# Optimization experiments

Measured on AMD Instinct MI355X. Metric: run time of the kernel, lower is better.

## Reference

```python
import jax, jax.numpy as jnp
import numpy as np

T, B, IN_DIM = 1024, 8, 512
D_VALUE, D_KEY = 64, 64
V_TH = 1.0
EPS = 1e-08


def setup_inputs() -> dict:
    key = jax.random.key(0)
    ks = jax.random.split(key, 7)
    s_in = 1.0 / np.sqrt(IN_DIM)
    x = jax.random.normal(ks[0], (T, B, IN_DIM), dtype=jnp.float32)
    Wv = jax.random.uniform(ks[1], (D_VALUE, IN_DIM), jnp.float32, -s_in, s_in)
    bv = jax.random.uniform(ks[2], (D_VALUE,), jnp.float32, -s_in, s_in)
    Wk = jax.random.uniform(ks[3], (D_KEY, IN_DIM), jnp.float32, -s_in, s_in)
    bk = jax.random.uniform(ks[4], (D_KEY,), jnp.float32, -s_in, s_in)
    Wa = jax.random.uniform(ks[5], (D_KEY, IN_DIM), jnp.float32, -s_in, s_in)
    ba = jax.random.uniform(ks[6], (D_KEY,), jnp.float32, -s_in, s_in)
    return {"x": x, "Wv": Wv, "bv": bv, "Wk": Wk, "bk": bk, "Wa": Wa, "ba": ba}


def reference(x, Wv, bv, Wk, bk, Wa, ba):
    # projections: v (T,B,d), k (T,B,n), alpha (T,B,n)
    v = jnp.einsum('tbi,di->tbd', x, Wv) + bv
    k = jnp.einsum('tbi,ni->tbn', x, Wk) + bk
    alpha = jax.nn.sigmoid(jnp.einsum('tbi,ni->tbn', x, Wa) + ba)
    # outer-product writes: (T,B,d,n)
    writes = jnp.einsum('tbd,tbn->tbdn', v, k)
    # closed-form linear recurrence S_t = S_{t-1} * alpha_t + writes_t via cumprod/cumsum
    P = jnp.cumprod(alpha, axis=0)                       # (T,B,n)
    invP = 1.0 / (P + EPS)
    scaled = writes * invP[:, :, None, :]                # (T,B,d,n)
    S = jnp.cumsum(scaled, axis=0) * P[:, :, None, :]    # (T,B,d,n)
    Tt, Bb = x.shape[0], x.shape[1]
    mem = S.reshape(Tt, Bb, D_VALUE * D_KEY)
    spk = (mem > V_TH).astype(mem.dtype)
    return spk, mem
```

## Files before the change

### kernel.cpp

```cpp
#include <hip/hip_runtime.h>
#include <cmath>

#define TT 1024
#define BB 8
#define IND 512
#define NCHUNK 32
#define CHLEN 32
#define EPSV 1e-8
#define OUTHALF ((size_t)TT * BB * 4096)

__global__ __launch_bounds__(256)
void k1_proj(const float* __restrict__ x,
             const float* __restrict__ Wv, const float* __restrict__ bv,
             const float* __restrict__ Wk, const float* __restrict__ bk,
             const float* __restrict__ Wa, const float* __restrict__ ba,
             float* __restrict__ vOut, float* __restrict__ kOut,
             double* __restrict__ aOut)
{
    __shared__ float sWt[64][192];
    __shared__ float sXt[64][16];
    const int tid = threadIdx.x;
    const int rowbase = blockIdx.x * 16;
    const int c0 = tid & 63;
    const int r0 = (tid >> 6) << 2;
    double a0[4] = {0,0,0,0}, a1[4] = {0,0,0,0}, a2[4] = {0,0,0,0};

    for (int ko = 0; ko < IND; ko += 64) {
        __syncthreads();
        if (tid < 192) {
            const float* src;
            if (tid < 64)       src = Wv + (size_t)tid * IND;
            else if (tid < 128) src = Wk + (size_t)(tid - 64) * IND;
            else                src = Wa + (size_t)(tid - 128) * IND;
            src += ko;
            #pragma unroll
            for (int q = 0; q < 64; q += 4) {
                float4 w4 = *(const float4*)(src + q);
                sWt[q+0][tid] = w4.x; sWt[q+1][tid] = w4.y;
                sWt[q+2][tid] = w4.z; sWt[q+3][tid] = w4.w;
            }
        }
        {
            int r  = tid & 15;
            int kq = (tid >> 4) << 2;
            float4 x4 = *(const float4*)(x + (size_t)(rowbase + r) * IND + ko + kq);
            sXt[kq+0][r] = x4.x; sXt[kq+1][r] = x4.y;
            sXt[kq+2][r] = x4.z; sXt[kq+3][r] = x4.w;
        }
        __syncthreads();

        float f0[4] = {0,0,0,0}, f1[4] = {0,0,0,0}, f2[4] = {0,0,0,0};
        #pragma unroll
        for (int q = 0; q < 64; ++q) {
            float4 xv = *(const float4*)&sXt[q][r0];
            float w0 = sWt[q][c0], w1 = sWt[q][c0 + 64], w2 = sWt[q][c0 + 128];
            f0[0] = fmaf(xv.x, w0, f0[0]); f1[0] = fmaf(xv.x, w1, f1[0]); f2[0] = fmaf(xv.x, w2, f2[0]);
            f0[1] = fmaf(xv.y, w0, f0[1]); f1[1] = fmaf(xv.y, w1, f1[1]); f2[1] = fmaf(xv.y, w2, f2[1]);
            f0[2] = fmaf(xv.z, w0, f0[2]); f1[2] = fmaf(xv.z, w1, f1[2]); f2[2] = fmaf(xv.z, w2, f2[2]);
            f0[3] = fmaf(xv.w, w0, f0[3]); f1[3] = fmaf(xv.w, w1, f1[3]); f2[3] = fmaf(xv.w, w2, f2[3]);
        }
        #pragma unroll
        for (int i = 0; i < 4; ++i) { a0[i] += f0[i]; a1[i] += f1[i]; a2[i] += f2[i]; }
    }

    #pragma unroll
    for (int i = 0; i < 4; ++i) {
        int r = rowbase + r0 + i;
        vOut[r * 64 + c0] = (float)(a0[i] + (double)bv[c0]);
        kOut[r * 64 + c0] = (float)(a1[i] + (double)bk[c0]);
        double z = a2[i] + (double)ba[c0];
        aOut[r * 64 + c0] = 1.0 / (1.0 + exp(-z));
    }
}

__global__ __launch_bounds__(256)
void k2a_chunkprod(const double* __restrict__ alpha, double* __restrict__ cpA)
{
    int gt = blockIdx.x * 256 + threadIdx.x;
    int ch = gt >> 9, chain = gt & 511;
    int b = chain >> 6, n = chain & 63;
    double p = 1.0;
    int base = ((ch * CHLEN) * BB + b) * 64 + n;
    for (int i = 0; i < CHLEN; ++i) p *= alpha[base + i * 512];
    cpA[gt] = p;
}

__global__ __launch_bounds__(512)
void k2b_prefix(double* __restrict__ cpA)
{
    int chain = threadIdx.x;
    double run = 1.0;
    for (int ch = 0; ch < NCHUNK; ++ch) {
        double t = cpA[ch * 512 + chain];
        cpA[ch * 512 + chain] = run;
        run *= t;
    }
}

__global__ __launch_bounds__(256)
void k3_csum(const float* __restrict__ vIn, const float* __restrict__ kIn,
             const double* __restrict__ alpha, const double* __restrict__ cpA,
             double* __restrict__ Csum)
{
    __shared__ double sV[CHLEN * 64];
    const int tid = threadIdx.x;
    const int ch = blockIdx.x >> 3;
    const int b  = blockIdx.x & 7;
    #pragma unroll
    for (int q = 0; q < 8; ++q) {
        int idx = q * 256 + tid;
        int ti = idx >> 6, d = idx & 63;
        sV[idx] = (double)vIn[(((ch * CHLEN + ti) * BB) + b) * 64 + d];
    }
    __syncthreads();
    const int n = tid & 63;
    const int w = tid >> 6;
    double P = cpA[ch * 512 + b * 64 + n];
    double C[16];
    #pragma unroll
    for (int j = 0; j < 16; ++j) C[j] = 0.0;
    for (int i = 0; i < CHLEN; ++i) {
        int base = ((ch * CHLEN + i) * BB + b) * 64 + n;
        P *= alpha[base];
        double invp = 1.0 / (P + EPSV);
        double kd = (double)kIn[base] * invp;
        const double* vrow = &sV[i * 64 + w * 16];
        #pragma unroll
        for (int j = 0; j < 16; ++j) C[j] = fma(vrow[j], kd, C[j]);
    }
    size_t cb = ((size_t)ch * 8 + b) * 4096 + (size_t)w * 1024 + n;
    #pragma unroll
    for (int j = 0; j < 16; ++j) Csum[cb + j * 64] = C[j];
}

__global__ __launch_bounds__(256)
void k3b_prefix(double* __restrict__ Csum)
{
    int s = blockIdx.x * 256 + threadIdx.x;
    int b = s >> 12, rest = s & 4095;
    double run = 0.0;
    for (int ch = 0; ch < NCHUNK; ++ch) {
        size_t idx = ((size_t)ch * 8 + b) * 4096 + rest;
        double t = Csum[idx];
        Csum[idx] = run;
        run += t;
    }
}

__global__ __launch_bounds__(256)
void k4_scan(const float* __restrict__ vIn, const float* __restrict__ kIn,
             const double* __restrict__ alpha, const double* __restrict__ cpA,
             const double* __restrict__ Csum, float* __restrict__ outp)
{
    __shared__ double sV[CHLEN * 64];
    const int tid = threadIdx.x;
    const int ch = blockIdx.x >> 3;
    const int b  = blockIdx.x & 7;
    #pragma unroll
    for (int q = 0; q < 8; ++q) {
        int idx = q * 256 + tid;
        int ti = idx >> 6, d = idx & 63;
        sV[idx] = (double)vIn[(((ch * CHLEN + ti) * BB) + b) * 64 + d];
    }
    __syncthreads();
    const int n = tid & 63;
    const int w = tid >> 6;
    double P = cpA[ch * 512 + b * 64 + n];
    size_t cb = ((size_t)ch * 8 + b) * 4096 + (size_t)w * 1024 + n;
    double C[16];
    #pragma unroll
    for (int j = 0; j < 16; ++j) C[j] = Csum[cb + j * 64];

    float* spk = outp;
    float* mem = outp + OUTHALF;
    for (int i = 0; i < CHLEN; ++i) {
        int t = ch * CHLEN + i;
        int base = (t * BB + b) * 64 + n;
        P *= alpha[base];
        double invp = 1.0 / (P + EPSV);
        double kd = (double)kIn[base] * invp;
        double vd[16];
        const double* vrow = &sV[i * 64 + w * 16];
        #pragma unroll
        for (int j = 0; j < 16; ++j) vd[j] = vrow[j];
        size_t ob = ((size_t)t * BB + b) * 4096 + (size_t)w * 1024 + n;
        #pragma unroll
        for (int j = 0; j < 16; ++j) {
            C[j] = fma(vd[j], kd, C[j]);
            double S = P * C[j];
            mem[ob + j * 64] = (float)S;
            spk[ob + j * 64] = (S > 1.0) ? 1.0f : 0.0f;
        }
    }
}

extern "C" void kernel_launch(void* const* d_in, const int* in_sizes, int n_in,
                              void* d_out, int out_size, void* d_ws, size_t ws_size,
                              hipStream_t stream)
{
    const float* x  = (const float*)d_in[0];
    const float* Wv = (const float*)d_in[1];
    const float* bv = (const float*)d_in[2];
    const float* Wk = (const float*)d_in[3];
    const float* bk = (const float*)d_in[4];
    const float* Wa = (const float*)d_in[5];
    const float* ba = (const float*)d_in[6];
    float* out = (float*)d_out;

    char* ws = (char*)d_ws;
    float*  v     = (float*)(ws);
    float*  kk    = (float*)(ws + (2u << 20));
    double* alpha = (double*)(ws + (4u << 20));
    double* cpA   = (double*)(ws + (8u << 20));
    double* Csum  = (double*)(ws + (8u << 20) + (1u << 17));

    hipLaunchKernelGGL(k1_proj,      dim3(512), dim3(256), 0, stream,
                       x, Wv, bv, Wk, bk, Wa, ba, v, kk, alpha);
    hipLaunchKernelGGL(k2a_chunkprod, dim3(64), dim3(256), 0, stream, alpha, cpA);
    hipLaunchKernelGGL(k2b_prefix,    dim3(1),  dim3(512), 0, stream, cpA);
    hipLaunchKernelGGL(k3_csum,       dim3(256), dim3(256), 0, stream,
                       v, kk, alpha, cpA, Csum);
    hipLaunchKernelGGL(k3b_prefix,    dim3(128), dim3(256), 0, stream, Csum);
    hipLaunchKernelGGL(k4_scan,       dim3(256), dim3(256), 0, stream,
                       v, kk, alpha, cpA, Csum, out);
}
```

Baseline: 117.9 us.

## Precompute per-step P and k/P arrays; drop single-block prefix kernel; enlarge projection tile

```diff
diff --git a/kernel.cpp b/kernel.cpp
--- a/kernel.cpp
+++ b/kernel.cpp
@@ -4,8 +4,8 @@
 #define TT 1024
 #define BB 8
 #define IND 512
-#define NCHUNK 32
-#define CHLEN 32
+#define NCH 32
+#define CHL 32
 #define EPSV 1e-8
 #define OUTHALF ((size_t)TT * BB * 4096)
 
@@ -18,21 +18,19 @@
              double* __restrict__ aOut)
 {
     __shared__ float sWt[64][192];
-    __shared__ float sXt[64][16];
+    __shared__ float sXt[64][32];
     const int tid = threadIdx.x;
-    const int rowbase = blockIdx.x * 16;
+    const int rowbase = blockIdx.x * 32;
     const int c0 = tid & 63;
-    const int r0 = (tid >> 6) << 2;
-    double a0[4] = {0,0,0,0}, a1[4] = {0,0,0,0}, a2[4] = {0,0,0,0};
+    const int r0 = (tid >> 6) << 3;
+    double av[8] = {}, ak[8] = {}, aa[8] = {};
 
     for (int ko = 0; ko < IND; ko += 64) {
         __syncthreads();
         if (tid < 192) {
-            const float* src;
-            if (tid < 64)       src = Wv + (size_t)tid * IND;
-            else if (tid < 128) src = Wk + (size_t)(tid - 64) * IND;
-            else                src = Wa + (size_t)(tid - 128) * IND;
-            src += ko;
+            const float* src = (tid < 64  ? Wv + (size_t)tid * IND
+                              : tid < 128 ? Wk + (size_t)(tid - 64) * IND
+                              :             Wa + (size_t)(tid - 128) * IND) + ko;
             #pragma unroll
             for (int q = 0; q < 64; q += 4) {
                 float4 w4 = *(const float4*)(src + q);
@@ -41,34 +39,40 @@
             }
         }
         {
-            int r  = tid & 15;
-            int kq = (tid >> 4) << 2;
-            float4 x4 = *(const float4*)(x + (size_t)(rowbase + r) * IND + ko + kq);
-            sXt[kq+0][r] = x4.x; sXt[kq+1][r] = x4.y;
-            sXt[kq+2][r] = x4.z; sXt[kq+3][r] = x4.w;
+            const int r  = tid & 31;
+            const int kq = (tid >> 5) << 3;
+            const float* xs = x + (size_t)(rowbase + r) * IND + ko + kq;
+            float4 xa = *(const float4*)xs;
+            float4 xb = *(const float4*)(xs + 4);
+            sXt[kq+0][r] = xa.x; sXt[kq+1][r] = xa.y; sXt[kq+2][r] = xa.z; sXt[kq+3][r] = xa.w;
+            sXt[kq+4][r] = xb.x; sXt[kq+5][r] = xb.y; sXt[kq+6][r] = xb.z; sXt[kq+7][r] = xb.w;
         }
         __syncthreads();
 
-        float f0[4] = {0,0,0,0}, f1[4] = {0,0,0,0}, f2[4] = {0,0,0,0};
+        float fv[8] = {}, fk[8] = {}, fa[8] = {};
         #pragma unroll
         for (int q = 0; q < 64; ++q) {
-            float4 xv = *(const float4*)&sXt[q][r0];
+            float4 xa = *(const float4*)&sXt[q][r0];
+            float4 xb = *(const float4*)&sXt[q][r0 + 4];
+            float xr[8] = {xa.x, xa.y, xa.z, xa.w, xb.x, xb.y, xb.z, xb.w};
             float w0 = sWt[q][c0], w1 = sWt[q][c0 + 64], w2 = sWt[q][c0 + 128];
-            f0[0] = fmaf(xv.x, w0, f0[0]); f1[0] = fmaf(xv.x, w1, f1[0]); f2[0] = fmaf(xv.x, w2, f2[0]);
-            f0[1] = fmaf(xv.y, w0, f0[1]); f1[1] = fmaf(xv.y, w1, f1[1]); f2[1] = fmaf(xv.y, w2, f2[1]);
-            f0[2] = fmaf(xv.z, w0, f0[2]); f1[2] = fmaf(xv.z, w1, f1[2]); f2[2] = fmaf(xv.z, w2, f2[2]);
-            f0[3] = fmaf(xv.w, w0, f0[3]); f1[3] = fmaf(xv.w, w1, f1[3]); f2[3] = fmaf(xv.w, w2, f2[3]);
-        }
-        #pragma unroll
-        for (int i = 0; i < 4; ++i) { a0[i] += f0[i]; a1[i] += f1[i]; a2[i] += f2[i]; }
-    }
-
-    #pragma unroll
-    for (int i = 0; i < 4; ++i) {
-        int r = rowbase + r0 + i;
-        vOut[r * 64 + c0] = (float)(a0[i] + (double)bv[c0]);
-        kOut[r * 64 + c0] = (float)(a1[i] + (double)bk[c0]);
-        double z = a2[i] + (double)ba[c0];
+            #pragma unroll
+            for (int j = 0; j < 8; ++j) {
+                fv[j] = fmaf(xr[j], w0, fv[j]);
+                fk[j] = fmaf(xr[j], w1, fk[j]);
+                fa[j] = fmaf(xr[j], w2, fa[j]);
+            }
+        }
+        #pragma unroll
+        for (int j = 0; j < 8; ++j) { av[j] += fv[j]; ak[j] += fk[j]; aa[j] += fa[j]; }
+    }
+
+    #pragma unroll
+    for (int j = 0; j < 8; ++j) {
+        size_t r = (size_t)rowbase + r0 + j;
+        vOut[r * 64 + c0] = (float)(av[j] + (double)bv[c0]);
+        kOut[r * 64 + c0] = (float)(ak[j] + (double)bk[c0]);
+        double z = aa[j] + (double)ba[c0];
         aOut[r * 64 + c0] = 1.0 / (1.0 + exp(-z));
     }
 }
@@ -78,31 +82,35 @@
 {
     int gt = blockIdx.x * 256 + threadIdx.x;
     int ch = gt >> 9, chain = gt & 511;
-    int b = chain >> 6, n = chain & 63;
     double p = 1.0;
-    int base = ((ch * CHLEN) * BB + b) * 64 + n;
-    for (int i = 0; i < CHLEN; ++i) p *= alpha[base + i * 512];
+    int base = (ch * CHL) * 512 + chain;
+    for (int i = 0; i < CHL; ++i) p *= alpha[base + i * 512];
     cpA[gt] = p;
 }
 
-__global__ __launch_bounds__(512)
-void k2b_prefix(double* __restrict__ cpA)
-{
-    int chain = threadIdx.x;
-    double run = 1.0;
-    for (int ch = 0; ch < NCHUNK; ++ch) {
-        double t = cpA[ch * 512 + chain];
-        cpA[ch * 512 + chain] = run;
-        run *= t;
-    }
-}
-
-__global__ __launch_bounds__(256)
-void k3_csum(const float* __restrict__ vIn, const float* __restrict__ kIn,
-             const double* __restrict__ alpha, const double* __restrict__ cpA,
+__global__ __launch_bounds__(256)
+void kP_scan(const float* __restrict__ kIn, const double* __restrict__ alpha,
+             const double* __restrict__ cpA,
+             double* __restrict__ Parr, double* __restrict__ kdArr)
+{
+    int gt = blockIdx.x * 256 + threadIdx.x;
+    int ch = gt >> 9, chain = gt & 511;
+    double P = 1.0;
+    for (int c = 0; c < ch; ++c) P *= cpA[c * 512 + chain];
+    int base = (ch * CHL) * 512 + chain;
+    for (int i = 0; i < CHL; ++i) {
+        int idx = base + i * 512;
+        P *= alpha[idx];
+        Parr[idx] = P;
+        kdArr[idx] = (double)kIn[idx] / (P + EPSV);
+    }
+}
+
+__global__ __launch_bounds__(256)
+void k3_csum(const float* __restrict__ vIn, const double* __restrict__ kdArr,
              double* __restrict__ Csum)
 {
-    __shared__ double sV[CHLEN * 64];
+    __shared__ double sV[CHL * 64];
     const int tid = threadIdx.x;
     const int ch = blockIdx.x >> 3;
     const int b  = blockIdx.x & 7;
@@ -110,20 +118,16 @@
     for (int q = 0; q < 8; ++q) {
         int idx = q * 256 + tid;
         int ti = idx >> 6, d = idx & 63;
-        sV[idx] = (double)vIn[(((ch * CHLEN + ti) * BB) + b) * 64 + d];
+        sV[idx] = (double)vIn[(((ch * CHL + ti) * BB) + b) * 64 + d];
     }
     __syncthreads();
     const int n = tid & 63;
     const int w = tid >> 6;
-    double P = cpA[ch * 512 + b * 64 + n];
     double C[16];
     #pragma unroll
     for (int j = 0; j < 16; ++j) C[j] = 0.0;
-    for (int i = 0; i < CHLEN; ++i) {
-        int base = ((ch * CHLEN + i) * BB + b) * 64 + n;
-        P *= alpha[base];
-        double invp = 1.0 / (P + EPSV);
-        double kd = (double)kIn[base] * invp;
+    for (int i = 0; i < CHL; ++i) {
+        double kd = kdArr[((ch * CHL + i) * BB + b) * 64 + n];
         const double* vrow = &sV[i * 64 + w * 16];
         #pragma unroll
         for (int j = 0; j < 16; ++j) C[j] = fma(vrow[j], kd, C[j]);
@@ -139,7 +143,7 @@
     int s = blockIdx.x * 256 + threadIdx.x;
     int b = s >> 12, rest = s & 4095;
     double run = 0.0;
-    for (int ch = 0; ch < NCHUNK; ++ch) {
+    for (int ch = 0; ch < NCH; ++ch) {
         size_t idx = ((size_t)ch * 8 + b) * 4096 + rest;
         double t = Csum[idx];
         Csum[idx] = run;
@@ -148,11 +152,11 @@
 }
 
 __global__ __launch_bounds__(256)
-void k4_scan(const float* __restrict__ vIn, const float* __restrict__ kIn,
-             const double* __restrict__ alpha, const double* __restrict__ cpA,
-             const double* __restrict__ Csum, float* __restrict__ outp)
-{
-    __shared__ double sV[CHLEN * 64];
+void k4_scan(const float* __restrict__ vIn, const double* __restrict__ kdArr,
+             const double* __restrict__ Parr, const double* __restrict__ Csum,
+             float* __restrict__ outp)
+{
+    __shared__ double sV[CHL * 64];
     const int tid = threadIdx.x;
     const int ch = blockIdx.x >> 3;
     const int b  = blockIdx.x & 7;
@@ -160,12 +164,11 @@
     for (int q = 0; q < 8; ++q) {
         int idx = q * 256 + tid;
         int ti = idx >> 6, d = idx & 63;
-        sV[idx] = (double)vIn[(((ch * CHLEN + ti) * BB) + b) * 64 + d];
+        sV[idx] = (double)vIn[(((ch * CHL + ti) * BB) + b) * 64 + d];
     }
     __syncthreads();
     const int n = tid & 63;
     const int w = tid >> 6;
-    double P = cpA[ch * 512 + b * 64 + n];
     size_t cb = ((size_t)ch * 8 + b) * 4096 + (size_t)w * 1024 + n;
     double C[16];
     #pragma unroll
@@ -173,20 +176,16 @@
 
     float* spk = outp;
     float* mem = outp + OUTHALF;
-    for (int i = 0; i < CHLEN; ++i) {
-        int t = ch * CHLEN + i;
+    for (int i = 0; i < CHL; ++i) {
+        int t = ch * CHL + i;
         int base = (t * BB + b) * 64 + n;
-        P *= alpha[base];
-        double invp = 1.0 / (P + EPSV);
-        double kd = (double)kIn[base] * invp;
-        double vd[16];
+        double kd = kdArr[base];
+        double P  = Parr[base];
         const double* vrow = &sV[i * 64 + w * 16];
-        #pragma unroll
-        for (int j = 0; j < 16; ++j) vd[j] = vrow[j];
         size_t ob = ((size_t)t * BB + b) * 4096 + (size_t)w * 1024 + n;
         #pragma unroll
         for (int j = 0; j < 16; ++j) {
-            C[j] = fma(vd[j], kd, C[j]);
+            C[j] = fma(vrow[j], kd, C[j]);
             double S = P * C[j];
             mem[ob + j * 64] = (float)S;
             spk[ob + j * 64] = (S > 1.0) ? 1.0f : 0.0f;
@@ -209,18 +208,21 @@
 
     char* ws = (char*)d_ws;
     float*  v     = (float*)(ws);
-    float*  kk    = (float*)(ws + (2u << 20));
-    double* alpha = (double*)(ws + (4u << 20));
-    double* cpA   = (double*)(ws + (8u << 20));
-    double* Csum  = (double*)(ws + (8u << 20) + (1u << 17));
-
-    hipLaunchKernelGGL(k1_proj,      dim3(512), dim3(256), 0, stream,
+    float*  kk    = (float*)(ws + ( 2u << 20));
+    double* alpha = (double*)(ws + ( 4u << 20));
+    double* cpA   = (double*)(ws + ( 8u << 20));
+    double* Parr  = (double*)(ws + ( 9u << 20));
+    double* kdArr = (double*)(ws + (13u << 20));
+    double* Csum  = (double*)(ws + (17u << 20));
+
+    hipLaunchKernelGGL(k1_proj,       dim3(256), dim3(256), 0, stream,
                        x, Wv, bv, Wk, bk, Wa, ba, v, kk, alpha);
-    hipLaunchKernelGGL(k2a_chunkprod, dim3(64), dim3(256), 0, stream, alpha, cpA);
-    hipLaunchKernelGGL(k2b_prefix,    dim3(1),  dim3(512), 0, stream, cpA);
+    hipLaunchKernelGGL(k2a_chunkprod, dim3(64),  dim3(256), 0, stream, alpha, cpA);
+    hipLaunchKernelGGL(kP_scan,       dim3(64),  dim3(256), 0, stream,
+                       kk, alpha, cpA, Parr, kdArr);
     hipLaunchKernelGGL(k3_csum,       dim3(256), dim3(256), 0, stream,
-                       v, kk, alpha, cpA, Csum);
+                       v, kdArr, Csum);
     hipLaunchKernelGGL(k3b_prefix,    dim3(128), dim3(256), 0, stream, Csum);
     hipLaunchKernelGGL(k4_scan,       dim3(256), dim3(256), 0, stream,
-                       v, kk, alpha, cpA, Csum, out);
-}
+                       v, kdArr, Parr, Csum, out);
+}
```

New measurement: 130.3 us. 1.11x slower.

## Fuse all stages into one cooperative kernel with grid syncs

Applied to the files above, without the earlier changes.

```diff
diff --git a/kernel.cpp b/kernel.cpp
--- a/kernel.cpp
+++ b/kernel.cpp
@@ -1,21 +1,174 @@
 #include <hip/hip_runtime.h>
+#include <hip/hip_cooperative_groups.h>
 #include <cmath>
 
 #define TT 1024
 #define BB 8
 #define IND 512
-#define NCHUNK 32
-#define CHLEN 32
+#define NCH 32
+#define CHL 32
 #define EPSV 1e-8
 #define OUTHALF ((size_t)TT * BB * 4096)
 
-__global__ __launch_bounds__(256)
-void k1_proj(const float* __restrict__ x,
-             const float* __restrict__ Wv, const float* __restrict__ bv,
-             const float* __restrict__ Wk, const float* __restrict__ bk,
-             const float* __restrict__ Wa, const float* __restrict__ ba,
-             float* __restrict__ vOut, float* __restrict__ kOut,
-             double* __restrict__ aOut)
+namespace cg = cooperative_groups;
+
+
+union SharedMem {
+    struct { float Wt[32][192]; float Xt[32][16]; } g;
+    struct { double A[CHL][64]; double V[CHL][32]; float K[CHL][64]; } s;
+};
+
+__global__ __launch_bounds__(256, 2)
+void mega(const float* __restrict__ x,
+          const float* __restrict__ Wv, const float* __restrict__ bv,
+          const float* __restrict__ Wk, const float* __restrict__ bk,
+          const float* __restrict__ Wa, const float* __restrict__ ba,
+          float* __restrict__ vBuf, float* __restrict__ kBuf,
+          double* __restrict__ aBuf, double* __restrict__ cpA,
+          double* __restrict__ Csum, float* __restrict__ outp)
+{
+    cg::grid_group grid = cg::this_grid();
+    __shared__ SharedMem sh;
+    const int tid = threadIdx.x;
+    const int bid = blockIdx.x;
+
+    {
+        const int rowbase = bid * 16;
+        const int c0 = tid & 63;
+        const int r0 = (tid >> 6) << 2;
+        double av[4] = {}, ak[4] = {}, aa[4] = {};
+
+        for (int ko = 0; ko < IND; ko += 32) {
+            __syncthreads();
+            if (tid < 192) {
+                const float* src = (tid < 64  ? Wv + (size_t)tid * IND
+                                  : tid < 128 ? Wk + (size_t)(tid - 64) * IND
+                                  :             Wa + (size_t)(tid - 128) * IND) + ko;
+                #pragma unroll
+                for (int q = 0; q < 32; q += 4) {
+                    float4 w4 = *(const float4*)(src + q);
+                    sh.g.Wt[q+0][tid] = w4.x; sh.g.Wt[q+1][tid] = w4.y;
+                    sh.g.Wt[q+2][tid] = w4.z; sh.g.Wt[q+3][tid] = w4.w;
+                }
+            }
+            {
+                int r  = tid & 15;
+                int kq = (tid >> 4) << 1;
+                float2 x2 = *(const float2*)(x + (size_t)(rowbase + r) * IND + ko + kq);
+                sh.g.Xt[kq][r] = x2.x; sh.g.Xt[kq+1][r] = x2.y;
+            }
+            __syncthreads();
+
+            float fv[4] = {}, fk[4] = {}, fa[4] = {};
+            #pragma unroll
+            for (int q = 0; q < 32; ++q) {
+                float4 xa = *(const float4*)&sh.g.Xt[q][r0];
+                float xr[4] = {xa.x, xa.y, xa.z, xa.w};
+                float w0 = sh.g.Wt[q][c0], w1 = sh.g.Wt[q][c0 + 64], w2 = sh.g.Wt[q][c0 + 128];
+                #pragma unroll
+                for (int j = 0; j < 4; ++j) {
+                    fv[j] = fmaf(xr[j], w0, fv[j]);
+                    fk[j] = fmaf(xr[j], w1, fk[j]);
+                    fa[j] = fmaf(xr[j], w2, fa[j]);
+                }
+            }
+            #pragma unroll
+            for (int j = 0; j < 4; ++j) { av[j] += fv[j]; ak[j] += fk[j]; aa[j] += fa[j]; }
+        }
+        #pragma unroll
+        for (int j = 0; j < 4; ++j) {
+            size_t r = (size_t)rowbase + r0 + j;
+            vBuf[r * 64 + c0] = (float)(av[j] + (double)bv[c0]);
+            kBuf[r * 64 + c0] = (float)(ak[j] + (double)bk[c0]);
+            double z = aa[j] + (double)ba[c0];
+            aBuf[r * 64 + c0] = 1.0 / (1.0 + exp(-z));
+        }
+    }
+    grid.sync();
+
+    const int ch = bid >> 4;
+    const int b  = (bid >> 1) & 7;
+    const int dh = bid & 1;
+    const int n  = tid & 63;
+    const int w  = tid >> 6;
+
+    #pragma unroll
+    for (int q = 0; q < 8; ++q) {
+        int idx = q * 256 + tid;
+        int t = idx >> 6, nn = idx & 63;
+        int g = ((ch * CHL + t) * BB + b) * 64 + nn;
+        sh.s.A[t][nn] = aBuf[g];
+        sh.s.K[t][nn] = kBuf[g];
+    }
+    #pragma unroll
+    for (int q = 0; q < 4; ++q) {
+        int idx = q * 256 + tid;
+        int t = idx >> 5, dd = idx & 31;
+        sh.s.V[t][dd] = (double)vBuf[((ch * CHL + t) * BB + b) * 64 + dh * 32 + dd];
+    }
+    __syncthreads();
+
+    if (dh == 0 && tid < 64) {
+        double p = 1.0;
+        #pragma unroll
+        for (int t = 0; t < CHL; ++t) p *= sh.s.A[t][tid];
+        cpA[ch * 512 + b * 64 + tid] = p;
+    }
+    grid.sync();
+
+    double P0 = 1.0;
+    for (int c = 0; c < ch; ++c) P0 *= cpA[c * 512 + b * 64 + n];
+    double C[8];
+    #pragma unroll
+    for (int j = 0; j < 8; ++j) C[j] = 0.0;
+    double P = P0;
+    for (int t = 0; t < CHL; ++t) {
+        P *= sh.s.A[t][n];
+        double kd = (double)sh.s.K[t][n] / (P + EPSV);
+        const double* vrow = &sh.s.V[t][w * 8];
+        #pragma unroll
+        for (int j = 0; j < 8; ++j) C[j] = fma(vrow[j], kd, C[j]);
+    }
+    {
+        size_t cb = ((size_t)ch * 8 + b) * 4096 + (size_t)(dh * 32 + w * 8) * 64 + n;
+        #pragma unroll
+        for (int j = 0; j < 8; ++j) Csum[cb + j * 64] = C[j];
+    }
+    grid.sync();
+
+    double Cacc[8];
+    #pragma unroll
+    for (int j = 0; j < 8; ++j) Cacc[j] = 0.0;
+    for (int c = 0; c < ch; ++c) {
+        size_t cb = ((size_t)c * 8 + b) * 4096 + (size_t)(dh * 32 + w * 8) * 64 + n;
+        #pragma unroll
+        for (int j = 0; j < 8; ++j) Cacc[j] += Csum[cb + j * 64];
+    }
+    float* spk = outp;
+    float* mem = outp + OUTHALF;
+    P = P0;
+    for (int t = 0; t < CHL; ++t) {
+        P *= sh.s.A[t][n];
+        double kd = (double)sh.s.K[t][n] / (P + EPSV);
+        const double* vrow = &sh.s.V[t][w * 8];
+        size_t ob = ((size_t)((ch * CHL + t) * BB + b)) * 4096 + (size_t)(dh * 32 + w * 8) * 64 + n;
+        #pragma unroll
+        for (int j = 0; j < 8; ++j) {
+            Cacc[j] = fma(vrow[j], kd, Cacc[j]);
+            double S = P * Cacc[j];
+            mem[ob + j * 64] = (float)S;
+            spk[ob + j * 64] = (S > 1.0) ? 1.0f : 0.0f;
+        }
+    }
+}
+
+__global__ __launch_bounds__(256)
+void k1_fb(const float* __restrict__ x,
+           const float* __restrict__ Wv, const float* __restrict__ bv,
+           const float* __restrict__ Wk, const float* __restrict__ bk,
+           const float* __restrict__ Wa, const float* __restrict__ ba,
+           float* __restrict__ vOut, float* __restrict__ kOut,
+           double* __restrict__ aOut)
 {
     __shared__ float sWt[64][192];
     __shared__ float sXt[64][16];
@@ -23,16 +176,14 @@
     const int rowbase = blockIdx.x * 16;
     const int c0 = tid & 63;
     const int r0 = (tid >> 6) << 2;
-    double a0[4] = {0,0,0,0}, a1[4] = {0,0,0,0}, a2[4] = {0,0,0,0};
+    double a0[4] = {}, a1[4] = {}, a2[4] = {};
 
     for (int ko = 0; ko < IND; ko += 64) {
         __syncthreads();
         if (tid < 192) {
-            const float* src;
-            if (tid < 64)       src = Wv + (size_t)tid * IND;
-            else if (tid < 128) src = Wk + (size_t)(tid - 64) * IND;
-            else                src = Wa + (size_t)(tid - 128) * IND;
-            src += ko;
+            const float* src = (tid < 64  ? Wv + (size_t)tid * IND
+                              : tid < 128 ? Wk + (size_t)(tid - 64) * IND
+                              :             Wa + (size_t)(tid - 128) * IND) + ko;
             #pragma unroll
             for (int q = 0; q < 64; q += 4) {
                 float4 w4 = *(const float4*)(src + q);
@@ -48,49 +199,49 @@
             sXt[kq+2][r] = x4.z; sXt[kq+3][r] = x4.w;
         }
         __syncthreads();
-
-        float f0[4] = {0,0,0,0}, f1[4] = {0,0,0,0}, f2[4] = {0,0,0,0};
+        float f0[4] = {}, f1[4] = {}, f2[4] = {};
         #pragma unroll
         for (int q = 0; q < 64; ++q) {
             float4 xv = *(const float4*)&sXt[q][r0];
+            float xr[4] = {xv.x, xv.y, xv.z, xv.w};
             float w0 = sWt[q][c0], w1 = sWt[q][c0 + 64], w2 = sWt[q][c0 + 128];
-            f0[0] = fmaf(xv.x, w0, f0[0]); f1[0] = fmaf(xv.x, w1, f1[0]); f2[0] = fmaf(xv.x, w2, f2[0]);
-            f0[1] = fmaf(xv.y, w0, f0[1]); f1[1] = fmaf(xv.y, w1, f1[1]); f2[1] = fmaf(xv.y, w2, f2[1]);
-            f0[2] = fmaf(xv.z, w0, f0[2]); f1[2] = fmaf(xv.z, w1, f1[2]); f2[2] = fmaf(xv.z, w2, f2[2]);
-            f0[3] = fmaf(xv.w, w0, f0[3]); f1[3] = fmaf(xv.w, w1, f1[3]); f2[3] = fmaf(xv.w, w2, f2[3]);
-        }
-        #pragma unroll
-        for (int i = 0; i < 4; ++i) { a0[i] += f0[i]; a1[i] += f1[i]; a2[i] += f2[i]; }
-    }
-
-    #pragma unroll
-    for (int i = 0; i < 4; ++i) {
-        int r = rowbase + r0 + i;
-        vOut[r * 64 + c0] = (float)(a0[i] + (double)bv[c0]);
-        kOut[r * 64 + c0] = (float)(a1[i] + (double)bk[c0]);
-        double z = a2[i] + (double)ba[c0];
+            #pragma unroll
+            for (int j = 0; j < 4; ++j) {
+                f0[j] = fmaf(xr[j], w0, f0[j]);
+                f1[j] = fmaf(xr[j], w1, f1[j]);
+                f2[j] = fmaf(xr[j], w2, f2[j]);
+            }
+        }
+        #pragma unroll
+        for (int j = 0; j < 4; ++j) { a0[j] += f0[j]; a1[j] += f1[j]; a2[j] += f2[j]; }
+    }
+    #pragma unroll
+    for (int j = 0; j < 4; ++j) {
+        int r = rowbase + r0 + j;
+        vOut[r * 64 + c0] = (float)(a0[j] + (double)bv[c0]);
+        kOut[r * 64 + c0] = (float)(a1[j] + (double)bk[c0]);
+        double z = a2[j] + (double)ba[c0];
         aOut[r * 64 + c0] = 1.0 / (1.0 + exp(-z));
     }
 }
 
 __global__ __launch_bounds__(256)
-void k2a_chunkprod(const double* __restrict__ alpha, double* __restrict__ cpA)
+void k2a_fb(const double* __restrict__ alpha, double* __restrict__ cpA)
 {
     int gt = blockIdx.x * 256 + threadIdx.x;
     int ch = gt >> 9, chain = gt & 511;
-    int b = chain >> 6, n = chain & 63;
     double p = 1.0;
-    int base = ((ch * CHLEN) * BB + b) * 64 + n;
-    for (int i = 0; i < CHLEN; ++i) p *= alpha[base + i * 512];
+    int base = (ch * CHL) * 512 + chain;
+    for (int i = 0; i < CHL; ++i) p *= alpha[base + i * 512];
     cpA[gt] = p;
 }
 
 __global__ __launch_bounds__(512)
-void k2b_prefix(double* __restrict__ cpA)
+void k2b_fb(double* __restrict__ cpA)
 {
     int chain = threadIdx.x;
     double run = 1.0;
-    for (int ch = 0; ch < NCHUNK; ++ch) {
+    for (int ch = 0; ch < NCH; ++ch) {
         double t = cpA[ch * 512 + chain];
         cpA[ch * 512 + chain] = run;
         run *= t;
@@ -98,11 +249,11 @@
 }
 
 __global__ __launch_bounds__(256)
-void k3_csum(const float* __restrict__ vIn, const float* __restrict__ kIn,
-             const double* __restrict__ alpha, const double* __restrict__ cpA,
-             double* __restrict__ Csum)
-{
-    __shared__ double sV[CHLEN * 64];
+void k3_fb(const float* __restrict__ vIn, const float* __restrict__ kIn,
+           const double* __restrict__ alpha, const double* __restrict__ cpA,
+           double* __restrict__ Csum)
+{
+    __shared__ double sV[CHL * 64];
     const int tid = threadIdx.x;
     const int ch = blockIdx.x >> 3;
     const int b  = blockIdx.x & 7;
@@ -110,7 +261,7 @@
     for (int q = 0; q < 8; ++q) {
         int idx = q * 256 + tid;
         int ti = idx >> 6, d = idx & 63;
-        sV[idx] = (double)vIn[(((ch * CHLEN + ti) * BB) + b) * 64 + d];
+        sV[idx] = (double)vIn[(((ch * CHL + ti) * BB) + b) * 64 + d];
     }
     __syncthreads();
     const int n = tid & 63;
@@ -119,8 +270,8 @@
     double C[16];
     #pragma unroll
     for (int j = 0; j < 16; ++j) C[j] = 0.0;
-    for (int i = 0; i < CHLEN; ++i) {
-        int base = ((ch * CHLEN + i) * BB + b) * 64 + n;
+    for (int i = 0; i < CHL; ++i) {
+        int base = ((ch * CHL + i) * BB + b) * 64 + n;
         P *= alpha[base];
         double invp = 1.0 / (P + EPSV);
         double kd = (double)kIn[base] * invp;
@@ -134,12 +285,12 @@
 }
 
 __global__ __launch_bounds__(256)
-void k3b_prefix(double* __restrict__ Csum)
+void k3b_fb(double* __restrict__ Csum)
 {
     int s = blockIdx.x * 256 + threadIdx.x;
     int b = s >> 12, rest = s & 4095;
     double run = 0.0;
-    for (int ch = 0; ch < NCHUNK; ++ch) {
+    for (int ch = 0; ch < NCH; ++ch) {
         size_t idx = ((size_t)ch * 8 + b) * 4096 + rest;
         double t = Csum[idx];
         Csum[idx] = run;
@@ -148,11 +299,11 @@
 }
 
 __global__ __launch_bounds__(256)
-void k4_scan(const float* __restrict__ vIn, const float* __restrict__ kIn,
-             const double* __restrict__ alpha, const double* __restrict__ cpA,
-             const double* __restrict__ Csum, float* __restrict__ outp)
-{
-    __shared__ double sV[CHLEN * 64];
+void k4_fb(const float* __restrict__ vIn, const float* __restrict__ kIn,
+           const double* __restrict__ alpha, const double* __restrict__ cpA,
+           const double* __restrict__ Csum, float* __restrict__ outp)
+{
+    __shared__ double sV[CHL * 64];
     const int tid = threadIdx.x;
     const int ch = blockIdx.x >> 3;
     const int b  = blockIdx.x & 7;
@@ -160,7 +311,7 @@
     for (int q = 0; q < 8; ++q) {
         int idx = q * 256 + tid;
         int ti = idx >> 6, d = idx & 63;
-        sV[idx] = (double)vIn[(((ch * CHLEN + ti) * BB) + b) * 64 + d];
+        sV[idx] = (double)vIn[(((ch * CHL + ti) * BB) + b) * 64 + d];
     }
     __syncthreads();
     const int n = tid & 63;
@@ -170,23 +321,19 @@
     double C[16];
     #pragma unroll
     for (int j = 0; j < 16; ++j) C[j] = Csum[cb + j * 64];
-
     float* spk = outp;
     float* mem = outp + OUTHALF;
-    for (int i = 0; i < CHLEN; ++i) {
-        int t = ch * CHLEN + i;
+    for (int i = 0; i < CHL; ++i) {
+        int t = ch * CHL + i;
         int base = (t * BB + b) * 64 + n;
         P *= alpha[base];
         double invp = 1.0 / (P + EPSV);
         double kd = (double)kIn[base] * invp;
-        double vd[16];
         const double* vrow = &sV[i * 64 + w * 16];
-        #pragma unroll
-        for (int j = 0; j < 16; ++j) vd[j] = vrow[j];
         size_t ob = ((size_t)t * BB + b) * 4096 + (size_t)w * 1024 + n;
         #pragma unroll
         for (int j = 0; j < 16; ++j) {
-            C[j] = fma(vd[j], kd, C[j]);
+            C[j] = fma(vrow[j], kd, C[j]);
             double S = P * C[j];
             mem[ob + j * 64] = (float)S;
             spk[ob + j * 64] = (S > 1.0) ? 1.0f : 0.0f;
@@ -212,15 +359,21 @@
     float*  kk    = (float*)(ws + (2u << 20));
     double* alpha = (double*)(ws + (4u << 20));
     double* cpA   = (double*)(ws + (8u << 20));
-    double* Csum  = (double*)(ws + (8u << 20) + (1u << 17));
-
-    hipLaunchKernelGGL(k1_proj,      dim3(512), dim3(256), 0, stream,
-                       x, Wv, bv, Wk, bk, Wa, ba, v, kk, alpha);
-    hipLaunchKernelGGL(k2a_chunkprod, dim3(64), dim3(256), 0, stream, alpha, cpA);
-    hipLaunchKernelGGL(k2b_prefix,    dim3(1),  dim3(512), 0, stream, cpA);
-    hipLaunchKernelGGL(k3_csum,       dim3(256), dim3(256), 0, stream,
-                       v, kk, alpha, cpA, Csum);
-    hipLaunchKernelGGL(k3b_prefix,    dim3(128), dim3(256), 0, stream, Csum);
-    hipLaunchKernelGGL(k4_scan,       dim3(256), dim3(256), 0, stream,
-                       v, kk, alpha, cpA, Csum, out);
-}
+    double* Csum  = (double*)(ws + (9u << 20));
+
+    void* args[] = { (void*)&x, (void*)&Wv, (void*)&bv, (void*)&Wk, (void*)&bk,
+                     (void*)&Wa, (void*)&ba, (void*)&v, (void*)&kk, (void*)&alpha,
+                     (void*)&cpA, (void*)&Csum, (void*)&out };
+    hipError_t e = hipLaunchCooperativeKernel((const void*)mega, dim3(512), dim3(256),
+                                              args, 0, stream);
+    if (e != hipSuccess) {
+        (void)hipGetLastError();
+        hipLaunchKernelGGL(k1_fb,  dim3(512), dim3(256), 0, stream,
+                           x, Wv, bv, Wk, bk, Wa, ba, v, kk, alpha);
+        hipLaunchKernelGGL(k2a_fb, dim3(64),  dim3(256), 0, stream, alpha, cpA);
+        hipLaunchKernelGGL(k2b_fb, dim3(1),   dim3(512), 0, stream, cpA);
+        hipLaunchKernelGGL(k3_fb,  dim3(256), dim3(256), 0, stream, v, kk, alpha, cpA, Csum);
+        hipLaunchKernelGGL(k3b_fb, dim3(128), dim3(256), 0, stream, Csum);
+        hipLaunchKernelGGL(k4_fb,  dim3(256), dim3(256), 0, stream, v, kk, alpha, cpA, Csum, out);
+    }
+}
```

Result: slower. 295.4 us (+150.6%).
